# Kernel tuning notes

Measured on AMD Instinct MI355X. Metric: run time of the kernel, lower is better.

Reference implementation:

```python
import jax, jax.numpy as jnp
import numpy as np

L, H, DIN, T, B = 3, 512, 512, 256, 64


def _lstm_layer(x, m, h0, c0, Wih, Whh, b, reverse):
    # x: [T,B,Din], m: [T,B,1], h0/c0: [B,H], Wih: [4H,Din], Whh: [4H,H], b: [4H]
    def step(carry, xm):
        h, c = carry
        xt, mt = xm
        gates = xt @ Wih.T + h @ Whh.T + b  # [B,4H]
        i, f, g, o = jnp.split(gates, 4, axis=-1)
        c_n = (jax.nn.sigmoid(f) * c + jax.nn.sigmoid(i) * jnp.tanh(g)) * mt
        h_n = jax.nn.sigmoid(o) * jnp.tanh(c_n) * mt
        return (h_n, c_n), h_n
    (hT, cT), hs = jax.lax.scan(step, (h0, c0), (x, m), reverse=reverse)
    return hs, hT, cT


def setup_inputs():
    key = jax.random.key(0)
    ks = jax.random.split(key, 16)
    s = 0.05
    return {
        "x": jax.random.normal(ks[0], (T, B, DIN), jnp.float32),
        "masks": (jax.random.uniform(ks[1], (T, B, 1)) < 0.9).astype(jnp.float32),
        "f_Wih0": jax.random.normal(ks[2], (4 * H, DIN), jnp.float32) * s,
        "f_Wih_rest": jax.random.normal(ks[3], (L - 1, 4 * H, 2 * H), jnp.float32) * s,
        "f_Whh": jax.random.normal(ks[4], (L, 4 * H, H), jnp.float32) * s,
        "f_b": jnp.zeros((L, 4 * H), jnp.float32),
        "b_Wih0": jax.random.normal(ks[5], (4 * H, DIN), jnp.float32) * s,
        "b_Wih_rest": jax.random.normal(ks[6], (L - 1, 4 * H, 2 * H), jnp.float32) * s,
        "b_Whh": jax.random.normal(ks[7], (L, 4 * H, H), jnp.float32) * s,
        "b_b": jnp.zeros((L, 4 * H), jnp.float32),
        "f_init": jax.random.normal(ks[8], (L, 2, H), jnp.float32) * s,
        "b_init": jax.random.normal(ks[9], (L, 2, H), jnp.float32) * s,
        "proj_W": jax.random.normal(ks[10], (L - 1, 2 * H, 2 * H), jnp.float32) * s,
        "proj_b": jnp.zeros((L - 1, 2 * H), jnp.float32),
    }


def reference(x, masks, f_Wih0, f_Wih_rest, f_Whh, f_b, b_Wih0, b_Wih_rest, b_Whh, b_b,
              f_init, b_init, proj_W, proj_b):
    batch = x.shape[1]
    inp = x
    h_n, c_n = [], []
    for layer in range(L):
        Wih_f = f_Wih0 if layer == 0 else f_Wih_rest[layer - 1]
        Wih_b = b_Wih0 if layer == 0 else b_Wih_rest[layer - 1]
        h0f = jnp.broadcast_to(f_init[layer, 0], (batch, H))
        c0f = jnp.broadcast_to(f_init[layer, 1], (batch, H))
        h0b = jnp.broadcast_to(b_init[layer, 0], (batch, H))
        c0b = jnp.broadcast_to(b_init[layer, 1], (batch, H))
        fout, fh, fc = _lstm_layer(inp, masks, h0f, c0f, Wih_f, f_Whh[layer], f_b[layer], False)
        bout, bh, bc = _lstm_layer(inp, masks, h0b, c0b, Wih_b, b_Whh[layer], b_b[layer], True)
        h_n += [fh, bh]
        c_n += [fc, bc]
        out = jnp.concatenate([fout, bout], axis=-1)  # [T,B,2H]
        if layer > 0:
            g = jax.nn.sigmoid(out @ proj_W[layer - 1].T + proj_b[layer - 1])
            out = g * out + (1.0 - g) * inp
        inp = out
    return out, jnp.stack(h_n, 0), jnp.stack(c_n, 0)
```

## Files before the change

### kernel.cpp

```cpp
#include <hip/hip_runtime.h>

typedef __attribute__((ext_vector_type(8))) short short8;
typedef __attribute__((ext_vector_type(4))) float f32x4;

#define MFMA_B16(a, b, c) __builtin_amdgcn_mfma_f32_16x16x32_bf16((a), (b), (c), 0, 0, 0)

#define TSTEPS 256
#define NBATCH 64
#define HID    512
#define NBLK   32
#define UB     16
#define HSLOT  (NBATCH * HID)

__device__ __forceinline__ unsigned short f2bf(float f) {
  unsigned int u = __float_as_uint(f);
  u += 0x7fffu + ((u >> 16) & 1u);
  return (unsigned short)(u >> 16);
}
__device__ __forceinline__ float bf2f(unsigned short s) {
  return __uint_as_float(((unsigned int)s) << 16);
}
__device__ __forceinline__ float sigm(float x) { return 1.0f / (1.0f + __expf(-x)); }
__device__ __forceinline__ float tanhf_(float x) {
  float xc = fminf(fmaxf(x, -15.0f), 15.0f);
  float e = __expf(2.0f * xc);
  return (e - 1.0f) / (e + 1.0f);
}

__device__ __forceinline__ short8 ld_llc16(const unsigned short* p) {
  union { unsigned long long q[2]; short8 s; } u;
  unsigned long long* a = (unsigned long long*)p;
  u.q[0] = __hip_atomic_load(a,     __ATOMIC_RELAXED, __HIP_MEMORY_SCOPE_AGENT);
  u.q[1] = __hip_atomic_load(a + 1, __ATOMIC_RELAXED, __HIP_MEMORY_SCOPE_AGENT);
  return u.s;
}

__device__ __forceinline__ void bar_arrive(unsigned int* cnt, unsigned int* gen) {
  asm volatile("s_waitcnt vmcnt(0)" ::: "memory");
  unsigned int old = __hip_atomic_fetch_add(cnt, 1u, __ATOMIC_RELAXED, __HIP_MEMORY_SCOPE_AGENT);
  if (((old + 1) & (NBLK - 1)) == 0u)
    __hip_atomic_store(gen, (old + 1) / NBLK, __ATOMIC_RELAXED, __HIP_MEMORY_SCOPE_AGENT);
}

__global__ void cvt_kernel(const float* __restrict__ src, unsigned short* __restrict__ dst, int n4) {
  int i = blockIdx.x * blockDim.x + threadIdx.x;
  int stride = gridDim.x * blockDim.x;
  for (; i < n4; i += stride) {
    f32x4 v = ((const f32x4*)src)[i];
    union { unsigned short u[4]; unsigned long long q; } o;
    o.u[0] = f2bf(v[0]); o.u[1] = f2bf(v[1]); o.u[2] = f2bf(v[2]); o.u[3] = f2bf(v[3]);
    ((unsigned long long*)dst)[i] = o.q;
  }
}

template<int K>
__global__ __launch_bounds__(256)
void gates_gemm(const unsigned short* __restrict__ act,
                const unsigned short* __restrict__ wcat,
                const float* __restrict__ bias_f,
                const float* __restrict__ bias_b,
                unsigned short* __restrict__ gates)
{
  const int lane = threadIdx.x & 63;
  const int wave = threadIdx.x >> 6;
  const int n = lane & 15, kb = lane >> 4;
  const int t = blockIdx.y;
  const int rbase = blockIdx.x * 256 + wave * 64;

  f32x4 acc[4][4];
  #pragma unroll
  for (int mt = 0; mt < 4; ++mt) {
    f32x4 bi;
    #pragma unroll
    for (int i = 0; i < 4; ++i) {
      int r = rbase + mt * 16 + kb * 4 + i;
      bi[i] = (r < 2048) ? bias_f[r] : bias_b[r - 2048];
    }
    #pragma unroll
    for (int nt = 0; nt < 4; ++nt) acc[mt][nt] = bi;
  }

  const unsigned short* wrow = wcat + (size_t)(rbase + n) * K + kb * 8;
  const unsigned short* arow = act + ((size_t)t * 64 + n) * K + kb * 8;
  #pragma unroll 4
  for (int ks = 0; ks < K / 32; ++ks) {
    short8 af[4], bf_[4];
    #pragma unroll
    for (int mt = 0; mt < 4; ++mt) af[mt] = *(const short8*)(wrow + (size_t)mt * 16 * K + ks * 32);
    #pragma unroll
    for (int nt = 0; nt < 4; ++nt) bf_[nt] = *(const short8*)(arow + (size_t)nt * 16 * K + ks * 32);
    #pragma unroll
    for (int mt = 0; mt < 4; ++mt)
      #pragma unroll
      for (int nt = 0; nt < 4; ++nt)
        acc[mt][nt] = MFMA_B16(af[mt], bf_[nt], acc[mt][nt]);
  }

  unsigned short* gbase = gates + (size_t)t * 4096 * 64;
  #pragma unroll
  for (int mt = 0; mt < 4; ++mt)
    #pragma unroll
    for (int i = 0; i < 4; ++i) {
      int r = rbase + mt * 16 + kb * 4 + i;
      #pragma unroll
      for (int nt = 0; nt < 4; ++nt)
        gbase[(size_t)r * 64 + nt * 16 + n] = f2bf(acc[mt][nt][i]);
    }
}

template<int DIN, int GXP>
__global__ __launch_bounds__(256, 1)
void scan_kernel(const unsigned short* __restrict__ act_in,
                 const unsigned short* __restrict__ gates,
                 unsigned short* __restrict__ act_out,
                 const unsigned short* __restrict__ wih_f,
                 const unsigned short* __restrict__ wih_b,
                 const unsigned short* __restrict__ whh_f,
                 const unsigned short* __restrict__ whh_b,
                 const float* __restrict__ bias_f,
                 const float* __restrict__ bias_b,
                 const float* __restrict__ init_f,
                 const float* __restrict__ init_b,
                 const float* __restrict__ masks,
                 unsigned short* hb,
                 unsigned int* bar,
                 float* out_h, float* out_c)
{
  const int bid  = blockIdx.x;
  const int dir  = bid >> 5;
  const int jb   = bid & (NBLK - 1);
  const int j0   = jb * UB;
  const int lane = threadIdx.x & 63;
  const int wave = threadIdx.x >> 6;
  const int n    = lane & 15;
  const int kb   = lane >> 4;
  const int u    = n & 7;
  const bool hif = (n >= 8);

  const unsigned short* wih = dir ? wih_b : wih_f;
  const unsigned short* whh = dir ? whh_b : whh_f;
  const float* bias = dir ? bias_b : bias_f;
  const float* init = dir ? init_b : init_f;
  unsigned int* cnt = bar + dir * 128;
  unsigned int* gen = cnt + 64;
  unsigned short* hbd = hb + dir * (2 * HSLOT);
  float* oh = out_h + dir * (NBATCH * HID);
  float* oc = out_c + dir * (NBATCH * HID);

  int wr[4];
  wr[0] = hif ? (512 + j0 + u) : (j0 + u);
  wr[1] = wr[0] + 8;
  wr[2] = wr[0] + 1024;
  wr[3] = wr[0] + 1032;

  float bb[4];
  const unsigned short* wihp[4];
  #pragma unroll
  for (int q = 0; q < 4; ++q) {
    bb[q] = bias[wr[q]];
    wihp[q] = wih + (size_t)wr[q] * DIN + kb * 8;
  }

  __shared__ short8 wlds[16 * 4 * 64];
  __shared__ unsigned short lsm[NBATCH * UB];

  for (int g = threadIdx.x; g < 4096; g += 256) {
    int n_ = g & 15, kb_ = (g >> 4) & 3, q_ = (g >> 6) & 3, ks_ = g >> 8;
    int grow = ((n_ >= 8) ? 512 : 0) + j0 + (n_ & 7) + (q_ & 1) * 8 + (q_ >> 1) * 1024;
    wlds[g] = *(const short8*)(whh + (size_t)grow * HID + ks_ * 32 + kb_ * 8);
  }

  if (wave == 0) {
    union { unsigned short us[16]; unsigned long long q[4]; } iv;
    #pragma unroll
    for (int k = 0; k < 16; ++k) iv.us[k] = f2bf(init[j0 + k]);
    unsigned long long* hd = (unsigned long long*)(hbd + jb * (NBATCH * UB) + lane * UB);
    #pragma unroll
    for (int k = 0; k < 4; ++k)
      __hip_atomic_store(hd + k, iv.q[k], __ATOMIC_RELAXED, __HIP_MEMORY_SCOPE_AGENT);
  }
  float cs[2][4];
  #pragma unroll
  for (int uh = 0; uh < 2; ++uh)
    #pragma unroll
    for (int i = 0; i < 4; ++i)
      cs[uh][i] = init[512 + j0 + uh * 8 + u];

  __syncthreads();
  if (threadIdx.x == 0) bar_arrive(cnt, gen);

  f32x4 acc_e[4], acc_o[4];

  auto wih_load = [&](int tstep) {
    #pragma unroll
    for (int q = 0; q < 4; ++q) {
      acc_e[q] = (f32x4){bb[q], bb[q], bb[q], bb[q]};
      acc_o[q] = (f32x4){0.f, 0.f, 0.f, 0.f};
    }
    const int tt2 = dir ? (TSTEPS - 1 - tstep) : tstep;
    const unsigned short* arow = act_in + ((size_t)tt2 * NBATCH + wave * 16 + n) * DIN + kb * 8;
    #pragma unroll
    for (int kt = 0; kt < DIN / 32; kt += 2) {
      short8 a0 = *(const short8*)(arow + kt * 32);
      short8 a1 = *(const short8*)(arow + kt * 32 + 32);
      #pragma unroll
      for (int q = 0; q < 4; ++q) {
        acc_e[q] = MFMA_B16(a0, *(const short8*)(wihp[q] + kt * 32), acc_e[q]);
        acc_o[q] = MFMA_B16(a1, *(const short8*)(wihp[q] + kt * 32 + 32), acc_o[q]);
      }
    }
  };

  if (!GXP) wih_load(0);

  for (int t = 0; t < TSTEPS; ++t) {
    const int tt = dir ? (TSTEPS - 1 - t) : t;

    if (GXP) {
      const unsigned short* gb = gates + ((size_t)tt * 4096 + dir * 2048) * 64 + wave * 16 + kb * 4;
      #pragma unroll
      for (int q = 0; q < 4; ++q) {
        union { unsigned long long q8; unsigned short us[4]; } gv;
        gv.q8 = *(const unsigned long long*)(gb + (size_t)wr[q] * 64);
        acc_e[q] = (f32x4){bf2f(gv.us[0]), bf2f(gv.us[1]), bf2f(gv.us[2]), bf2f(gv.us[3])};
        acc_o[q] = (f32x4){0.f, 0.f, 0.f, 0.f};
      }
    }

    if (threadIdx.x == 0) {
      while (__hip_atomic_load(gen, __ATOMIC_RELAXED, __HIP_MEMORY_SCOPE_AGENT) < (unsigned int)(t + 1))
        __builtin_amdgcn_s_sleep(1);
    }
    __syncthreads();

    {
      const unsigned short* hrow = hbd + (t & 1) * HSLOT
                                 + (kb >> 1) * 1024 + (kb & 1) * 8 + (wave * 16 + n) * UB;
      short8 hf[16];
      #pragma unroll
      for (int ks = 0; ks < 16; ++ks) hf[ks] = ld_llc16(hrow + ks * 2048);
      #pragma unroll
      for (int ks = 0; ks < 16; ++ks) {
        f32x4* ac = (ks & 1) ? acc_o : acc_e;
        #pragma unroll
        for (int q = 0; q < 4; ++q)
          ac[q] = MFMA_B16(hf[ks], wlds[(ks * 4 + q) * 64 + lane], ac[q]);
      }
    }

    f32x4 mk = *(const f32x4*)(masks + tt * NBATCH + wave * 16 + kb * 4);

    #pragma unroll
    for (int uh = 0; uh < 2; ++uh) {
      f32x4 aif = acc_e[uh] + acc_o[uh];
      f32x4 ago = acc_e[2 + uh] + acc_o[2 + uh];
      f32x4 oif, ogo;
      #pragma unroll
      for (int r = 0; r < 4; ++r) {
        oif[r] = __shfl_xor(aif[r], 8, 64);
        ogo[r] = __shfl_xor(ago[r], 8, 64);
      }
      #pragma unroll
      for (int i = 0; i < 4; ++i) {
        float vi = hif ? oif[i] : aif[i];
        float vf = hif ? aif[i] : oif[i];
        float vg = hif ? ogo[i] : ago[i];
        float vo = hif ? ago[i] : ogo[i];
        float cn = (sigm(vf) * cs[uh][i] + sigm(vi) * tanhf_(vg)) * mk[i];
        float hvv = sigm(vo) * tanhf_(cn) * mk[i];
        cs[uh][i] = cn;
        if (!hif) {
          const int b = wave * 16 + kb * 4 + i;
          lsm[b * UB + uh * 8 + u] = f2bf(hvv);
          if (t == TSTEPS - 1) {
            oh[b * HID + j0 + uh * 8 + u] = hvv;
            oc[b * HID + j0 + uh * 8 + u] = cn;
          }
        }
      }
    }

    __syncthreads();

    if (wave == 0) {
      const unsigned long long* lq = (const unsigned long long*)lsm;
      unsigned long long q0 = lq[lane * 4 + 0];
      unsigned long long q1 = lq[lane * 4 + 1];
      unsigned long long q2 = lq[lane * 4 + 2];
      unsigned long long q3 = lq[lane * 4 + 3];
      unsigned short* hnxt = hbd + ((t + 1) & 1) * HSLOT;
      unsigned long long* hd = (unsigned long long*)(hnxt + jb * (NBATCH * UB) + lane * UB);
      __hip_atomic_store(hd + 0, q0, __ATOMIC_RELAXED, __HIP_MEMORY_SCOPE_AGENT);
      __hip_atomic_store(hd + 1, q1, __ATOMIC_RELAXED, __HIP_MEMORY_SCOPE_AGENT);
      __hip_atomic_store(hd + 2, q2, __ATOMIC_RELAXED, __HIP_MEMORY_SCOPE_AGENT);
      __hip_atomic_store(hd + 3, q3, __ATOMIC_RELAXED, __HIP_MEMORY_SCOPE_AGENT);
      union { unsigned long long q[2]; short8 s; } p0, p1;
      p0.q[0] = q0; p0.q[1] = q1; p1.q[0] = q2; p1.q[1] = q3;
      short8* ar = (short8*)(act_out + ((size_t)tt * NBATCH + lane) * (2 * HID) + dir * HID + j0);
      ar[0] = p0.s;
      ar[1] = p1.s;
    }
    if (threadIdx.x == 0) bar_arrive(cnt, gen);

    if (!GXP && t + 1 < TSTEPS) wih_load(t + 1);
  }
}

template<int FINAL>
__global__ __launch_bounds__(256)
void highway_kernel(const unsigned short* __restrict__ raw,
                    unsigned short* __restrict__ inp,
                    const unsigned short* __restrict__ pw,
                    const float* __restrict__ pb,
                    float* __restrict__ outf)
{
  const int lane = threadIdx.x & 63;
  const int wave = threadIdx.x >> 6;
  const int n = lane & 15, kb = lane >> 4;
  const int r0 = blockIdx.x * 64 + wave * 16;
  const int c0 = blockIdx.y * 64;

  f32x4 acc[4];
  #pragma unroll
  for (int nt = 0; nt < 4; ++nt) {
    float b = pb[c0 + nt * 16 + n];
    acc[nt] = (f32x4){b, b, b, b};
  }
  const unsigned short* arow = raw + (r0 + n) * 1024 + kb * 8;
  #pragma unroll 4
  for (int kt = 0; kt < 32; ++kt) {
    short8 a = *(const short8*)(arow + kt * 32);
    #pragma unroll
    for (int nt = 0; nt < 4; ++nt) {
      short8 b = *(const short8*)(pw + (c0 + nt * 16 + n) * 1024 + kt * 32 + kb * 8);
      acc[nt] = MFMA_B16(a, b, acc[nt]);
    }
  }
  #pragma unroll
  for (int nt = 0; nt < 4; ++nt) {
    #pragma unroll
    for (int i = 0; i < 4; ++i) {
      int row = r0 + kb * 4 + i;
      int col = c0 + nt * 16 + n;
      float g = sigm(acc[nt][i]);
      float rv = bf2f(raw[row * 1024 + col]);
      float iv = bf2f(inp[row * 1024 + col]);
      float ov = g * rv + (1.0f - g) * iv;
      if (FINAL) outf[row * 1024 + col] = ov;
      else       inp[row * 1024 + col] = f2bf(ov);
    }
  }
}

extern "C" void kernel_launch(void* const* d_in, const int* in_sizes, int n_in,
                              void* d_out, int out_size, void* d_ws, size_t ws_size,
                              hipStream_t stream) {
  const float* x     = (const float*)d_in[0];
  const float* masks = (const float*)d_in[1];
  const float* fWih0 = (const float*)d_in[2];
  const float* fWihR = (const float*)d_in[3];
  const float* fWhh  = (const float*)d_in[4];
  const float* fb    = (const float*)d_in[5];
  const float* bWih0 = (const float*)d_in[6];
  const float* bWihR = (const float*)d_in[7];
  const float* bWhh  = (const float*)d_in[8];
  const float* bbias = (const float*)d_in[9];
  const float* fInit = (const float*)d_in[10];
  const float* bInit = (const float*)d_in[11];
  const float* projW = (const float*)d_in[12];
  const float* projB = (const float*)d_in[13];
  float* out = (float*)d_out;

  char* ws = (char*)d_ws;
  unsigned short* bufA  = (unsigned short*)(ws + 0);
  unsigned short* bufB  = (unsigned short*)(ws + 33554432);
  unsigned short* xbf   = (unsigned short*)(ws + 67108864);
  unsigned short* wcat0 = (unsigned short*)(ws + 83886080);
  unsigned short* wcat1 = (unsigned short*)(ws + 88080384);
  unsigned short* wcat2 = (unsigned short*)(ws + 96468992);
  unsigned short* whf   = (unsigned short*)(ws + 104857600);
  unsigned short* whb   = (unsigned short*)(ws + 111149056);
  unsigned short* pj    = (unsigned short*)(ws + 117440512);
  unsigned short* hbuf  = (unsigned short*)(ws + 121634816);
  unsigned int*   bar   = (unsigned int*)(ws + 121896960);
  unsigned short* gates = (unsigned short*)(ws + 121901056);
  const bool gx = ws_size >= 256118784ull;

  hipMemsetAsync(bar, 0, 4096, stream);

  cvt_kernel<<<1024, 256, 0, stream>>>(x,     xbf,   (256*64*512)  / 4);
  cvt_kernel<<<1024, 256, 0, stream>>>(fWih0, wcat0,              (2048*512)  / 4);
  cvt_kernel<<<1024, 256, 0, stream>>>(bWih0, wcat0 + 2048*512,   (2048*512)  / 4);
  cvt_kernel<<<1024, 256, 0, stream>>>(fWihR,             wcat1,             (2048*1024) / 4);
  cvt_kernel<<<1024, 256, 0, stream>>>(bWihR,             wcat1 + 2048*1024, (2048*1024) / 4);
  cvt_kernel<<<1024, 256, 0, stream>>>(fWihR + 2048*1024, wcat2,             (2048*1024) / 4);
  cvt_kernel<<<1024, 256, 0, stream>>>(bWihR + 2048*1024, wcat2 + 2048*1024, (2048*1024) / 4);
  cvt_kernel<<<1024, 256, 0, stream>>>(fWhh,  whf,   (3*2048*512)  / 4);
  cvt_kernel<<<1024, 256, 0, stream>>>(bWhh,  whb,   (3*2048*512)  / 4);
  cvt_kernel<<<1024, 256, 0, stream>>>(projW, pj,    (2*1024*1024) / 4);

  float* outH = out + 16777216;
  float* outC = out + 16777216 + 6*64*512;

  if (gx) {
    gates_gemm<512><<<dim3(16, 256), 256, 0, stream>>>(xbf, wcat0, fb, bbias, gates);
    scan_kernel<512, 1><<<64, 256, 0, stream>>>(
        xbf, gates, bufA,
        wcat0, wcat0 + 2048*512, whf, whb,
        fb, bbias, fInit, bInit, masks, hbuf, bar,
        outH, outC);
    gates_gemm<1024><<<dim3(16, 256), 256, 0, stream>>>(bufA, wcat1, fb + 2048, bbias + 2048, gates);
    scan_kernel<1024, 1><<<64, 256, 0, stream>>>(
        bufA, gates, bufB,
        wcat1, wcat1 + 2048*1024, whf + 2048*512, whb + 2048*512,
        fb + 2048, bbias + 2048, fInit + 1024, bInit + 1024, masks, hbuf, bar + 256,
        outH + 2*64*512, outC + 2*64*512);
    highway_kernel<0><<<dim3(256, 16), 256, 0, stream>>>(bufB, bufA, pj, projB, nullptr);
    gates_gemm<1024><<<dim3(16, 256), 256, 0, stream>>>(bufA, wcat2, fb + 2*2048, bbias + 2*2048, gates);
    scan_kernel<1024, 1><<<64, 256, 0, stream>>>(
        bufA, gates, bufB,
        wcat2, wcat2 + 2048*1024, whf + 2*2048*512, whb + 2*2048*512,
        fb + 2*2048, bbias + 2*2048, fInit + 2048, bInit + 2048, masks, hbuf, bar + 512,
        outH + 4*64*512, outC + 4*64*512);
    highway_kernel<1><<<dim3(256, 16), 256, 0, stream>>>(bufB, bufA, pj + 1024*1024, projB + 1024, out);
  } else {
    scan_kernel<512, 0><<<64, 256, 0, stream>>>(
        xbf, nullptr, bufA,
        wcat0, wcat0 + 2048*512, whf, whb,
        fb, bbias, fInit, bInit, masks, hbuf, bar,
        outH, outC);
    scan_kernel<1024, 0><<<64, 256, 0, stream>>>(
        bufA, nullptr, bufB,
        wcat1, wcat1 + 2048*1024, whf + 2048*512, whb + 2048*512,
        fb + 2048, bbias + 2048, fInit + 1024, bInit + 1024, masks, hbuf, bar + 256,
        outH + 2*64*512, outC + 2*64*512);
    highway_kernel<0><<<dim3(256, 16), 256, 0, stream>>>(bufB, bufA, pj, projB, nullptr);
    scan_kernel<1024, 0><<<64, 256, 0, stream>>>(
        bufA, nullptr, bufB,
        wcat2, wcat2 + 2048*1024, whf + 2*2048*512, whb + 2*2048*512,
        fb + 2*2048, bbias + 2*2048, fInit + 2048, bInit + 2048, masks, hbuf, bar + 512,
        outH + 4*64*512, outC + 4*64*512);
    highway_kernel<1><<<dim3(256, 16), 256, 0, stream>>>(bufB, bufA, pj + 1024*1024, projB + 1024, out);
  }
}
```

Before: 6.505 ms.

## Replace counter barrier with per-block step flags and double gates GEMM timestep reuse

```diff
diff --git a/kernel.cpp b/kernel.cpp
--- a/kernel.cpp
+++ b/kernel.cpp
@@ -33,13 +33,6 @@
   u.q[0] = __hip_atomic_load(a,     __ATOMIC_RELAXED, __HIP_MEMORY_SCOPE_AGENT);
   u.q[1] = __hip_atomic_load(a + 1, __ATOMIC_RELAXED, __HIP_MEMORY_SCOPE_AGENT);
   return u.s;
-}
-
-__device__ __forceinline__ void bar_arrive(unsigned int* cnt, unsigned int* gen) {
-  asm volatile("s_waitcnt vmcnt(0)" ::: "memory");
-  unsigned int old = __hip_atomic_fetch_add(cnt, 1u, __ATOMIC_RELAXED, __HIP_MEMORY_SCOPE_AGENT);
-  if (((old + 1) & (NBLK - 1)) == 0u)
-    __hip_atomic_store(gen, (old + 1) / NBLK, __ATOMIC_RELAXED, __HIP_MEMORY_SCOPE_AGENT);
 }
 
 __global__ void cvt_kernel(const float* __restrict__ src, unsigned short* __restrict__ dst, int n4) {
@@ -64,10 +57,10 @@
   const int lane = threadIdx.x & 63;
   const int wave = threadIdx.x >> 6;
   const int n = lane & 15, kb = lane >> 4;
-  const int t = blockIdx.y;
+  const int t0 = blockIdx.y * 2;
   const int rbase = blockIdx.x * 256 + wave * 64;
 
-  f32x4 acc[4][4];
+  f32x4 acc[2][4][4];
   #pragma unroll
   for (int mt = 0; mt < 4; ++mt) {
     f32x4 bi;
@@ -77,35 +70,44 @@
       bi[i] = (r < 2048) ? bias_f[r] : bias_b[r - 2048];
     }
     #pragma unroll
-    for (int nt = 0; nt < 4; ++nt) acc[mt][nt] = bi;
-  }
-
-  const unsigned short* wrow = wcat + (size_t)(rbase + n) * K + kb * 8;
-  const unsigned short* arow = act + ((size_t)t * 64 + n) * K + kb * 8;
-  #pragma unroll 4
+    for (int nt = 0; nt < 4; ++nt) { acc[0][mt][nt] = bi; acc[1][mt][nt] = bi; }
+  }
+
+  const unsigned short* wrow  = wcat + (size_t)(rbase + n) * K + kb * 8;
+  const unsigned short* arow0 = act + ((size_t)t0 * 64 + n) * K + kb * 8;
+  const unsigned short* arow1 = arow0 + (size_t)64 * K;
+  #pragma unroll 2
   for (int ks = 0; ks < K / 32; ++ks) {
-    short8 af[4], bf_[4];
+    short8 af[4], b0[4], b1[4];
     #pragma unroll
     for (int mt = 0; mt < 4; ++mt) af[mt] = *(const short8*)(wrow + (size_t)mt * 16 * K + ks * 32);
     #pragma unroll
-    for (int nt = 0; nt < 4; ++nt) bf_[nt] = *(const short8*)(arow + (size_t)nt * 16 * K + ks * 32);
+    for (int nt = 0; nt < 4; ++nt) {
+      b0[nt] = *(const short8*)(arow0 + (size_t)nt * 16 * K + ks * 32);
+      b1[nt] = *(const short8*)(arow1 + (size_t)nt * 16 * K + ks * 32);
+    }
     #pragma unroll
     for (int mt = 0; mt < 4; ++mt)
       #pragma unroll
-      for (int nt = 0; nt < 4; ++nt)
-        acc[mt][nt] = MFMA_B16(af[mt], bf_[nt], acc[mt][nt]);
-  }
-
-  unsigned short* gbase = gates + (size_t)t * 4096 * 64;
-  #pragma unroll
-  for (int mt = 0; mt < 4; ++mt)
-    #pragma unroll
-    for (int i = 0; i < 4; ++i) {
-      int r = rbase + mt * 16 + kb * 4 + i;
-      #pragma unroll
-      for (int nt = 0; nt < 4; ++nt)
-        gbase[(size_t)r * 64 + nt * 16 + n] = f2bf(acc[mt][nt][i]);
-    }
+      for (int nt = 0; nt < 4; ++nt) {
+        acc[0][mt][nt] = MFMA_B16(af[mt], b0[nt], acc[0][mt][nt]);
+        acc[1][mt][nt] = MFMA_B16(af[mt], b1[nt], acc[1][mt][nt]);
+      }
+  }
+
+  #pragma unroll
+  for (int t2 = 0; t2 < 2; ++t2) {
+    unsigned short* gbase = gates + (size_t)(t0 + t2) * 4096 * 64;
+    #pragma unroll
+    for (int mt = 0; mt < 4; ++mt)
+      #pragma unroll
+      for (int i = 0; i < 4; ++i) {
+        int r = rbase + mt * 16 + kb * 4 + i;
+        #pragma unroll
+        for (int nt = 0; nt < 4; ++nt)
+          gbase[(size_t)r * 64 + nt * 16 + n] = f2bf(acc[t2][mt][nt][i]);
+      }
+  }
 }
 
 template<int DIN, int GXP>
@@ -123,7 +125,7 @@
                  const float* __restrict__ init_b,
                  const float* __restrict__ masks,
                  unsigned short* hb,
-                 unsigned int* bar,
+                 unsigned int* flags,
                  float* out_h, float* out_c)
 {
   const int bid  = blockIdx.x;
@@ -141,8 +143,8 @@
   const unsigned short* whh = dir ? whh_b : whh_f;
   const float* bias = dir ? bias_b : bias_f;
   const float* init = dir ? init_b : init_f;
-  unsigned int* cnt = bar + dir * 128;
-  unsigned int* gen = cnt + 64;
+  unsigned int* fbase  = flags + dir * (NBLK * 32);
+  unsigned int* myflag = fbase + jb * 32;
   unsigned short* hbd = hb + dir * (2 * HSLOT);
   float* oh = out_h + dir * (NBATCH * HID);
   float* oc = out_c + dir * (NBATCH * HID);
@@ -187,7 +189,11 @@
       cs[uh][i] = init[512 + j0 + uh * 8 + u];
 
   __syncthreads();
-  if (threadIdx.x == 0) bar_arrive(cnt, gen);
+  if (wave == 0) {
+    asm volatile("s_waitcnt vmcnt(0)" ::: "memory");
+    if (lane == 0)
+      __hip_atomic_store(myflag, 1u, __ATOMIC_RELAXED, __HIP_MEMORY_SCOPE_AGENT);
+  }
 
   f32x4 acc_e[4], acc_o[4];
 
@@ -216,6 +222,7 @@
   for (int t = 0; t < TSTEPS; ++t) {
     const int tt = dir ? (TSTEPS - 1 - t) : t;
 
+    f32x4 mk = *(const f32x4*)(masks + tt * NBATCH + wave * 16 + kb * 4);
     if (GXP) {
       const unsigned short* gb = gates + ((size_t)tt * 4096 + dir * 2048) * 64 + wave * 16 + kb * 4;
       #pragma unroll
@@ -227,8 +234,10 @@
       }
     }
 
-    if (threadIdx.x == 0) {
-      while (__hip_atomic_load(gen, __ATOMIC_RELAXED, __HIP_MEMORY_SCOPE_AGENT) < (unsigned int)(t + 1))
+    if (wave == 0) {
+      const unsigned int tgt = t + 1;
+      unsigned int* fp = fbase + (lane & 31) * 32;
+      while (!__all((int)(__hip_atomic_load(fp, __ATOMIC_RELAXED, __HIP_MEMORY_SCOPE_AGENT) >= tgt)))
         __builtin_amdgcn_s_sleep(1);
     }
     __syncthreads();
@@ -247,8 +256,6 @@
           ac[q] = MFMA_B16(hf[ks], wlds[(ks * 4 + q) * 64 + lane], ac[q]);
       }
     }
-
-    f32x4 mk = *(const f32x4*)(masks + tt * NBATCH + wave * 16 + kb * 4);
 
     #pragma unroll
     for (int uh = 0; uh < 2; ++uh) {
@@ -288,19 +295,23 @@
       unsigned long long q1 = lq[lane * 4 + 1];
       unsigned long long q2 = lq[lane * 4 + 2];
       unsigned long long q3 = lq[lane * 4 + 3];
-      unsigned short* hnxt = hbd + ((t + 1) & 1) * HSLOT;
-      unsigned long long* hd = (unsigned long long*)(hnxt + jb * (NBATCH * UB) + lane * UB);
-      __hip_atomic_store(hd + 0, q0, __ATOMIC_RELAXED, __HIP_MEMORY_SCOPE_AGENT);
-      __hip_atomic_store(hd + 1, q1, __ATOMIC_RELAXED, __HIP_MEMORY_SCOPE_AGENT);
-      __hip_atomic_store(hd + 2, q2, __ATOMIC_RELAXED, __HIP_MEMORY_SCOPE_AGENT);
-      __hip_atomic_store(hd + 3, q3, __ATOMIC_RELAXED, __HIP_MEMORY_SCOPE_AGENT);
+      if (t + 1 < TSTEPS) {
+        unsigned short* hnxt = hbd + ((t + 1) & 1) * HSLOT;
+        unsigned long long* hd = (unsigned long long*)(hnxt + jb * (NBATCH * UB) + lane * UB);
+        __hip_atomic_store(hd + 0, q0, __ATOMIC_RELAXED, __HIP_MEMORY_SCOPE_AGENT);
+        __hip_atomic_store(hd + 1, q1, __ATOMIC_RELAXED, __HIP_MEMORY_SCOPE_AGENT);
+        __hip_atomic_store(hd + 2, q2, __ATOMIC_RELAXED, __HIP_MEMORY_SCOPE_AGENT);
+        __hip_atomic_store(hd + 3, q3, __ATOMIC_RELAXED, __HIP_MEMORY_SCOPE_AGENT);
+        asm volatile("s_waitcnt vmcnt(0)" ::: "memory");
+        if (lane == 0)
+          __hip_atomic_store(myflag, (unsigned int)(t + 2), __ATOMIC_RELAXED, __HIP_MEMORY_SCOPE_AGENT);
+      }
       union { unsigned long long q[2]; short8 s; } p0, p1;
       p0.q[0] = q0; p0.q[1] = q1; p1.q[0] = q2; p1.q[1] = q3;
       short8* ar = (short8*)(act_out + ((size_t)tt * NBATCH + lane) * (2 * HID) + dir * HID + j0);
       ar[0] = p0.s;
       ar[1] = p1.s;
     }
-    if (threadIdx.x == 0) bar_arrive(cnt, gen);
 
     if (!GXP && t + 1 < TSTEPS) wih_load(t + 1);
   }
@@ -383,10 +394,10 @@
   unsigned short* pj    = (unsigned short*)(ws + 117440512);
   unsigned short* hbuf  = (unsigned short*)(ws + 121634816);
   unsigned int*   bar   = (unsigned int*)(ws + 121896960);
-  unsigned short* gates = (unsigned short*)(ws + 121901056);
-  const bool gx = ws_size >= 256118784ull;
-
-  hipMemsetAsync(bar, 0, 4096, stream);
+  unsigned short* gates = (unsigned short*)(ws + 121921536);
+  const bool gx = ws_size >= 256139264ull;
+
+  hipMemsetAsync(bar, 0, 24576, stream);
 
   cvt_kernel<<<1024, 256, 0, stream>>>(x,     xbf,   (256*64*512)  / 4);
   cvt_kernel<<<1024, 256, 0, stream>>>(fWih0, wcat0,              (2048*512)  / 4);
@@ -403,24 +414,24 @@
   float* outC = out + 16777216 + 6*64*512;
 
   if (gx) {
-    gates_gemm<512><<<dim3(16, 256), 256, 0, stream>>>(xbf, wcat0, fb, bbias, gates);
+    gates_gemm<512><<<dim3(16, 128), 256, 0, stream>>>(xbf, wcat0, fb, bbias, gates);
     scan_kernel<512, 1><<<64, 256, 0, stream>>>(
         xbf, gates, bufA,
         wcat0, wcat0 + 2048*512, whf, whb,
         fb, bbias, fInit, bInit, masks, hbuf, bar,
         outH, outC);
-    gates_gemm<1024><<<dim3(16, 256), 256, 0, stream>>>(bufA, wcat1, fb + 2048, bbias + 2048, gates);
+    gates_gemm<1024><<<dim3(16, 128), 256, 0, stream>>>(bufA, wcat1, fb + 2048, bbias + 2048, gates);
     scan_kernel<1024, 1><<<64, 256, 0, stream>>>(
         bufA, gates, bufB,
         wcat1, wcat1 + 2048*1024, whf + 2048*512, whb + 2048*512,
-        fb + 2048, bbias + 2048, fInit + 1024, bInit + 1024, masks, hbuf, bar + 256,
+        fb + 2048, bbias + 2048, fInit + 1024, bInit + 1024, masks, hbuf, bar + 2048,
         outH + 2*64*512, outC + 2*64*512);
     highway_kernel<0><<<dim3(256, 16), 256, 0, stream>>>(bufB, bufA, pj, projB, nullptr);
-    gates_gemm<1024><<<dim3(16, 256), 256, 0, stream>>>(bufA, wcat2, fb + 2*2048, bbias + 2*2048, gates);
+    gates_gemm<1024><<<dim3(16, 128), 256, 0, stream>>>(bufA, wcat2, fb + 2*2048, bbias + 2*2048, gates);
     scan_kernel<1024, 1><<<64, 256, 0, stream>>>(
         bufA, gates, bufB,
         wcat2, wcat2 + 2048*1024, whf + 2*2048*512, whb + 2*2048*512,
-        fb + 2*2048, bbias + 2*2048, fInit + 2048, bInit + 2048, masks, hbuf, bar + 512,
+        fb + 2*2048, bbias + 2*2048, fInit + 2048, bInit + 2048, masks, hbuf, bar + 4096,
         outH + 4*64*512, outC + 4*64*512);
     highway_kernel<1><<<dim3(256, 16), 256, 0, stream>>>(bufB, bufA, pj + 1024*1024, projB + 1024, out);
   } else {
@@ -432,13 +443,13 @@
     scan_kernel<1024, 0><<<64, 256, 0, stream>>>(
         bufA, nullptr, bufB,
         wcat1, wcat1 + 2048*1024, whf + 2048*512, whb + 2048*512,
-        fb + 2048, bbias + 2048, fInit + 1024, bInit + 1024, masks, hbuf, bar + 256,
+        fb + 2048, bbias + 2048, fInit + 1024, bInit + 1024, masks, hbuf, bar + 2048,
         outH + 2*64*512, outC + 2*64*512);
     highway_kernel<0><<<dim3(256, 16), 256, 0, stream>>>(bufB, bufA, pj, projB, nullptr);
     scan_kernel<1024, 0><<<64, 256, 0, stream>>>(
         bufA, nullptr, bufB,
         wcat2, wcat2 + 2048*1024, whf + 2*2048*512, whb + 2*2048*512,
-        fb + 2*2048, bbias + 2*2048, fInit + 2048, bInit + 2048, masks, hbuf, bar + 512,
+        fb + 2*2048, bbias + 2*2048, fInit + 2048, bInit + 2048, masks, hbuf, bar + 4096,
         outH + 4*64*512, outC + 4*64*512);
     highway_kernel<1><<<dim3(256, 16), 256, 0, stream>>>(bufB, bufA, pj + 1024*1024, projB + 1024, out);
   }
```

New measurement: 5.992 ms. 7.9% less time.
